# Performance work log

Measured on AMD Instinct MI355X. Metric: run time of the kernel, lower is better.

The kernel has to match this reference:

```python
import jax, jax.numpy as jnp
import numpy as np
import math

B, S, D, H = 1, 2048, 2048, 16
DH, DHID, DKER = 128, 256, 128  # dim_head, dim_hid, dim_ker


def _uniform(k, shape, a):
    return jax.random.uniform(k, shape, jnp.float32, -a, a)


def setup_inputs() -> dict:
    key = jax.random.key(0)
    ks = jax.random.split(key, 14)
    a1 = math.sqrt(6.0 / (DH + DHID))
    a2 = math.sqrt(6.0 / (DKER + DHID))
    a3 = math.sqrt(6.0 / (2 * DKER))
    return {
        "x_t": jax.random.normal(ks[0], (B, S, D), jnp.float32),
        "q": jax.random.normal(ks[1], (B, S, D), jnp.float32),
        "k": jax.random.normal(ks[2], (B, S, D), jnp.float32),
        "v": jax.random.normal(ks[3], (B, S, D), jnp.float32),
        "lr_attn_mask": jax.random.bernoulli(ks[4], 0.5, (B, H, S, S)),
        "sparse_norms_lse": jax.random.normal(ks[5], (B, H, S, 1), jnp.float32),
        "sparse_attn_weights": jax.random.normal(ks[6], (B, H, S, S), jnp.float32),
        "lambda_constant": 0,
        "kernel_q_mat1": _uniform(ks[7], (H, DH, DHID), a1),
        "kernel_k_mat1": _uniform(ks[8], (H, DH, DHID), a1),
        "kernel_q_mat2": _uniform(ks[9], (H, DHID, DKER), a2),
        "kernel_k_mat2": _uniform(ks[10], (H, DHID, DKER), a2),
        "interaction_k": _uniform(ks[11], (H, DKER, DKER), a3),
        "scalingD": jnp.full((1, H, 1, DKER), 1e-4, jnp.float32),
        "scalingD2": jnp.full((1, H, 1, DKER), 1e-4, jnp.float32),
    }


def _gelu(x):
    return jax.nn.gelu(x, approximate=False)  # matches torch F.gelu default


def reference(x_t, q, k, v, lr_attn_mask, sparse_norms_lse, sparse_attn_weights,
              lambda_constant, kernel_q_mat1, kernel_k_mat1, kernel_q_mat2,
              kernel_k_mat2, interaction_k, scalingD, scalingD2):
    Bq, Sq, Dq = q.shape
    dh = Dq // H
    # [B,S,D] -> [B,H,S,dh]
    qh = q.reshape(Bq, Sq, H, dh).transpose(0, 2, 1, 3)
    kh = k.reshape(Bq, Sq, H, dh).transpose(0, 2, 1, 3)
    vh = v.reshape(Bq, Sq, H, dh).transpose(0, 2, 1, 3)

    # per-head two-layer feature maps (dropout is identity at eval)
    qf = _gelu(jnp.einsum('bhsd,hde->bhse', qh, kernel_q_mat1))
    qf = _gelu(jnp.einsum('bhse,hef->bhsf', qf, kernel_q_mat2))
    kf = _gelu(jnp.einsum('bhsd,hde->bhse', kh, kernel_k_mat1))
    kf = jnp.abs(scalingD) * _gelu(jnp.einsum('bhse,hef->bhsf', kf, kernel_k_mat2))
    kf = kf + jnp.einsum('bhse,hef->bhsf', kf, interaction_k) * scalingD2

    # masked non-negative kernel scores [B,H,S,S]
    scores = jnp.einsum('bhse,bhte->bhst', jnp.abs(qf), jnp.abs(kf))
    m = lr_attn_mask.astype(scores.dtype)
    scores = m * scores

    lr_norms_lse = jnp.log(scores.sum(axis=-1, keepdims=True) + 1e-6)
    norm_factor_lse = jnp.logaddexp(lr_norms_lse, sparse_norms_lse)

    logits = jnp.log(scores + 1e-6) * m + (1.0 - m) * sparse_attn_weights
    attn = jnp.exp(logits - norm_factor_lse)

    out = jnp.einsum('bhst,bhtd->bhsd', attn, vh)
    return out.transpose(0, 2, 1, 3).reshape(Bq, Sq, Dq)
```

## Files before the change

### kernel.cpp

```cpp
#include <hip/hip_runtime.h>
#include <hip/hip_bf16.h>
#include <math.h>

#define H_    16
#define S_    2048
#define D_    2048
#define DH_   128
#define DHID_ 256
#define DKER_ 128

typedef __attribute__((ext_vector_type(8))) short short8v;
typedef __attribute__((ext_vector_type(4))) float float4v;
typedef __attribute__((ext_vector_type(4))) int int4v;

static __device__ __forceinline__ short f2bf(float x){
  union { float f; unsigned u; } v; v.f = x;
  unsigned r = v.u + 0x7fffu + ((v.u >> 16) & 1u);
  return (short)(r >> 16);
}
static __device__ __forceinline__ float gelu_f(float x){
  float y = 0.7978845608028654f * (x + 0.044715f * x * x * x);
  float e = __expf(2.0f * y);
  float t = 1.0f - 2.0f / (e + 1.0f);
  return 0.5f * x * (1.0f + t);
}
static __device__ __forceinline__ float4v mfma16(short8v a, short8v b, float4v c){
  return __builtin_amdgcn_mfma_f32_16x16x32_bf16(a, b, c, 0, 0, 0);
}
static __device__ __forceinline__ unsigned cvtpk(float lo, float hi){
  unsigned d;
  asm("v_cvt_pk_bf16_f32 %0, %1, %2" : "=v"(d) : "v"(lo), "v"(hi));
  return d;
}
static __device__ __forceinline__ void glds16(const void* g, void* l){
  __builtin_amdgcn_global_load_lds(
      (const __attribute__((address_space(1))) void*)g,
      (__attribute__((address_space(3))) void*)l, 16, 0, 0);
}

__global__ __launch_bounds__(256) void prep_kernel(
    const void* __restrict__ mask,
    unsigned* __restrict__ MP,
    const float* __restrict__ w1q, short* __restrict__ W1qT,
    const float* __restrict__ w1k, short* __restrict__ W1kT,
    const float* __restrict__ w2q, short* __restrict__ W2qT,
    const float* __restrict__ w2k, short* __restrict__ W2kT,
    const float* __restrict__ ik,  short* __restrict__ IKT,
    const float* __restrict__ v,   short* __restrict__ V2){
  __shared__ float tile[32][33];
  __shared__ int sb, sf, so, sflag;
  int b = blockIdx.x;
  int tid = threadIdx.x;

  if (b < 8192){
    {
      const unsigned* mw = (const unsigned*)mask;
      int bin = 1, f32ok = 1, odd0 = 1;
      for (int i = tid; i < 1024; i += 256){
        unsigned w = mw[i];
        if (w > 1u) bin = 0;
        if (w != 0u && w != 0x3F800000u) f32ok = 0;
        if ((i & 1) && w != 0u) odd0 = 0;
      }
      if (tid == 0){ sb = 1; sf = 1; so = 1; }
      __syncthreads();
      if (!bin)  atomicAnd(&sb, 0);
      if (!f32ok) atomicAnd(&sf, 0);
      if (!odd0) atomicAnd(&so, 0);
      __syncthreads();
      if (tid == 0) sflag = sb ? (so ? 3 : 0) : (sf ? 2 : 1);
      __syncthreads();
    }
    int flag = sflag;
    size_t w = (size_t)b * 256 + tid;
    size_t base = w * 32;
    unsigned bits = 0;
    if (flag == 0){
      const int4v* m = (const int4v*)((const int*)mask + base);
      #pragma unroll
      for (int c = 0; c < 8; ++c){
        int4v x = m[c];
        bits |= (x[0] != 0 ? 1u : 0u) << (c*4+0);
        bits |= (x[1] != 0 ? 1u : 0u) << (c*4+1);
        bits |= (x[2] != 0 ? 1u : 0u) << (c*4+2);
        bits |= (x[3] != 0 ? 1u : 0u) << (c*4+3);
      }
    } else if (flag == 1){
      const int4v* m = (const int4v*)((const unsigned char*)mask + base);
      #pragma unroll
      for (int c = 0; c < 2; ++c){
        int4v x = m[c];
        #pragma unroll
        for (int e = 0; e < 4; ++e){
          unsigned u = (unsigned)x[e];
          #pragma unroll
          for (int bb = 0; bb < 4; ++bb)
            bits |= (((u >> (8*bb)) & 0xffu) != 0 ? 1u : 0u) << (c*16 + e*4 + bb);
        }
      }
    } else if (flag == 2){
      const float4v* m = (const float4v*)((const float*)mask + base);
      #pragma unroll
      for (int c = 0; c < 8; ++c){
        float4v x = m[c];
        bits |= (x[0] != 0.0f ? 1u : 0u) << (c*4+0);
        bits |= (x[1] != 0.0f ? 1u : 0u) << (c*4+1);
        bits |= (x[2] != 0.0f ? 1u : 0u) << (c*4+2);
        bits |= (x[3] != 0.0f ? 1u : 0u) << (c*4+3);
      }
    } else {
      const int4v* m = (const int4v*)((const int*)mask + 2*base);
      #pragma unroll
      for (int c = 0; c < 16; ++c){
        int4v x = m[c];
        bits |= (x[0] != 0 ? 1u : 0u) << (c*2+0);
        bits |= (x[2] != 0 ? 1u : 0u) << (c*2+1);
      }
    }
    MP[w] = bits;
    return;
  }
  b -= 8192;
  if (b < 2048){
    int h = b >> 7, bx = b & 127;
    int d = tid & 127, oct = tid >> 7;
    int t8 = bx * 2 + oct;
    int t32 = t8 >> 2, o = t8 & 3;
    const float* src = v + (size_t)(t32 * 32) * D_ + h * DH_ + d;
    short8v ov;
    #pragma unroll
    for (int j = 0; j < 8; ++j){
      int trel = o * 4 + (j & 3) + ((j >> 2) << 4);
      ov[j] = f2bf(src[(size_t)trel * D_]);
    }
    *(short8v*)(V2 + (((size_t)h * (S_/8) + t8) * DH_ + d) * 8) = ov;
    return;
  }
  b -= 2048;
  const float* src; short* dst; int R, C, bx, by, h;
  if (b < 512){        src = w1q; dst = W1qT; R = DH_;  C = DHID_;
                       bx = b & 7; by = (b >> 3) & 3; h = b >> 5; }
  else if (b < 1024){  b -= 512;  src = w1k; dst = W1kT; R = DH_;  C = DHID_;
                       bx = b & 7; by = (b >> 3) & 3; h = b >> 5; }
  else if (b < 1536){  b -= 1024; src = w2q; dst = W2qT; R = DHID_; C = DKER_;
                       bx = b & 3; by = (b >> 2) & 7; h = b >> 5; }
  else if (b < 2048){  b -= 1536; src = w2k; dst = W2kT; R = DHID_; C = DKER_;
                       bx = b & 3; by = (b >> 2) & 7; h = b >> 5; }
  else {               b -= 2048; src = ik;  dst = IKT;  R = DKER_; C = DKER_;
                       bx = b & 3; by = (b >> 2) & 3; h = b >> 4; }
  int tx = tid & 31, ty = tid >> 5;
  int c0 = bx * 32, r0 = by * 32;
  const float* s = src + (size_t)h * R * C;
  short* d = dst + (size_t)h * R * C;
  #pragma unroll
  for (int i = 0; i < 32; i += 8)
    tile[ty + i][tx] = s[(size_t)(r0 + ty + i) * C + (c0 + tx)];
  __syncthreads();
  #pragma unroll
  for (int i = 0; i < 32; i += 8)
    d[(size_t)(c0 + ty + i) * R + (r0 + tx)] = f2bf(tile[tx][ty + i]);
}

__global__ __launch_bounds__(256) void feat_kernel(
    const float* __restrict__ q, const float* __restrict__ k,
    const short* __restrict__ W1qT, const short* __restrict__ W2qT,
    const short* __restrict__ W1kT, const short* __restrict__ W2kT,
    const short* __restrict__ IKT, const float* __restrict__ sD,
    const float* __restrict__ sD2,
    short* __restrict__ QF, short* __restrict__ KF){
  __shared__ __align__(16) short yls[4][16][264];
  int z = blockIdx.y;
  bool isq = z < 16;
  int h = z & 15;
  const float* X = isq ? q : k;
  const short* W1T = isq ? W1qT : W1kT;
  const short* W2T = isq ? W2qT : W2kT;
  int lane = threadIdx.x & 63, warp = threadIdx.x >> 6;
  int s0 = (blockIdx.x * 4 + warp) * 16;
  int col = lane & 15, rg = lane >> 4;
  short8v a[4];
  {
    const float* xr = X + (size_t)(s0 + col) * D_ + h * DH_;
    #pragma unroll
    for (int kb = 0; kb < 4; ++kb){
      int k0 = kb * 32 + rg * 8;
      float4v x0 = *(const float4v*)(xr + k0);
      float4v x1 = *(const float4v*)(xr + k0 + 4);
      union { unsigned u[4]; short8v v8; } t;
      t.u[0] = cvtpk(x0[0], x0[1]); t.u[1] = cvtpk(x0[2], x0[3]);
      t.u[2] = cvtpk(x1[0], x1[1]); t.u[3] = cvtpk(x1[2], x1[3]);
      a[kb] = t.v8;
    }
  }
  const short* wbase = W1T + (size_t)h * DHID_ * DH_;
  #pragma unroll
  for (int j = 0; j < 16; ++j){
    int n = j * 16;
    float4v c = {0.f, 0.f, 0.f, 0.f};
    const short* wr = wbase + (size_t)(n + col) * DH_ + rg * 8;
    #pragma unroll
    for (int kb = 0; kb < 4; ++kb)
      c = mfma16(a[kb], *(const short8v*)(wr + kb * 32), c);
    #pragma unroll
    for (int r = 0; r < 4; ++r)
      yls[warp][rg * 4 + r][n + col] = f2bf(gelu_f(c[r]));
  }
  short8v a2[8];
  #pragma unroll
  for (int kb = 0; kb < 8; ++kb)
    a2[kb] = *(const short8v*)(&yls[warp][col][kb * 32 + rg * 8]);
  const short* wb2 = W2T + (size_t)h * DKER_ * DHID_;

  if (isq){
    short* qb = QF + ((size_t)h * S_ + s0) * DKER_;
    #pragma unroll
    for (int j = 0; j < 8; ++j){
      int n = j * 16;
      float4v c = {0.f, 0.f, 0.f, 0.f};
      const short* wr = wb2 + (size_t)(n + col) * DHID_ + rg * 8;
      #pragma unroll
      for (int kb = 0; kb < 8; ++kb)
        c = mfma16(a2[kb], *(const short8v*)(wr + kb * 32), c);
      #pragma unroll
      for (int r = 0; r < 4; ++r)
        qb[(size_t)(rg * 4 + r) * DKER_ + n + col] = f2bf(fabsf(gelu_f(c[r])));
    }
    return;
  }
  float kf0[8][4];
  #pragma unroll
  for (int j = 0; j < 8; ++j){
    int n = j * 16;
    float4v c = {0.f, 0.f, 0.f, 0.f};
    const short* wr = wb2 + (size_t)(n + col) * DHID_ + rg * 8;
    #pragma unroll
    for (int kb = 0; kb < 8; ++kb)
      c = mfma16(a2[kb], *(const short8v*)(wr + kb * 32), c);
    float sc = fabsf(sD[h * DKER_ + n + col]);
    #pragma unroll
    for (int r = 0; r < 4; ++r) kf0[j][r] = sc * gelu_f(c[r]);
  }
  #pragma unroll
  for (int j = 0; j < 8; ++j)
    #pragma unroll
    for (int r = 0; r < 4; ++r)
      yls[warp][rg * 4 + r][j * 16 + col] = f2bf(kf0[j][r]);
  short8v pa[4];
  #pragma unroll
  for (int kb = 0; kb < 4; ++kb)
    pa[kb] = *(const short8v*)(&yls[warp][col][kb * 32 + rg * 8]);
  const short* ib = IKT + (size_t)h * DKER_ * DKER_;
  short* ko = KF + ((size_t)h * S_ + s0) * DKER_;
  #pragma unroll
  for (int j = 0; j < 8; ++j){
    int n = j * 16;
    float4v c = {0.f, 0.f, 0.f, 0.f};
    const short* ir = ib + (size_t)(n + col) * DKER_ + rg * 8;
    #pragma unroll
    for (int kb = 0; kb < 4; ++kb)
      c = mfma16(pa[kb], *(const short8v*)(ir + kb * 32), c);
    float s2 = sD2[h * DKER_ + n + col];
    #pragma unroll
    for (int r = 0; r < 4; ++r)
      ko[(size_t)(rg * 4 + r) * DKER_ + n + col] = f2bf(fabsf(kf0[j][r] + c[r] * s2));
  }
}

__global__ __launch_bounds__(512, 4) void main_attn_kernel(
    const short* __restrict__ QF, const short* __restrict__ KF,
    const short* __restrict__ V2, const unsigned* __restrict__ MP,
    const float* __restrict__ SW, const float* __restrict__ LSE,
    float* __restrict__ OUT){
  __shared__ __align__(16) char smem[65536];
  int tid = threadIdx.x;
  int lane = tid & 63, warp = tid >> 6;
  int hf = warp >> 2, w4 = warp & 3;
  int flat = blockIdx.y * 32 + blockIdx.x;
  int nf = (flat & 7) * 64 + (flat >> 3);
  int sblk = nf & 31, h = nf >> 5;
  int tbase = hf * (S_ / 2);
  int s0 = (sblk * 4 + w4) * 16;
  int col = lane & 15, rg = lane >> 4;

  short* kbuf = (short*)(smem + hf * 32768);
  short* vbuf = (short*)(smem + hf * 32768 + 16384);

  short8v qa[4];
  const short* qr = QF + ((size_t)h * S_ + s0 + col) * DKER_ + rg * 8;
  #pragma unroll
  for (int kb = 0; kb < 4; ++kb) qa[kb] = *(const short8v*)(qr + kb * 32);

  float4v acc[8];
  #pragma unroll
  for (int j = 0; j < 8; ++j) acc[j] = (float4v){0.f, 0.f, 0.f, 0.f};
  float rs = 0.f;

  const char* kf_base = (const char*)(KF + ((size_t)h * S_ + tbase) * DKER_);
  const char* v2_base = (const char*)(V2 + ((size_t)h * (S_/8) + (tbase >> 3)) * DH_ * 8);
  int c0 = w4 * 64 + lane, c1 = c0 + 256;
  int kg0 = (c0 * 16) ^ (((c0 >> 4) & 7) << 4);
  int kg1 = (c1 * 16) ^ (((c1 >> 4) & 7) << 4);
  int vg0 = c0 * 16, vg1 = c1 * 16;
  int lds_lo = w4 * 512, lds_hi = 2048 + w4 * 512;

  const float* swrow = SW + ((size_t)h * S_ + s0 + col) * S_ + tbase + rg * 4;
  const unsigned* mpr = MP + ((size_t)h * S_ + s0 + col) * (S_ / 32) + (tbase >> 5);

  {
    glds16(kf_base + kg0, &kbuf[lds_lo]);
    glds16(kf_base + kg1, &kbuf[lds_hi]);
    glds16(v2_base + vg0, &vbuf[lds_lo]);
    glds16(v2_base + vg1, &vbuf[lds_hi]);
  }
  __syncthreads();

  int swz = (col & 7) << 4;
  int rowb0 = col * 256 + rg * 16;
  const int NITER = (S_ / 2) / 32;

  for (int ti = 0; ti < NITER; ++ti){
    int cur = ti & 1;
    if (ti + 1 < NITER){
      const char* kt = kf_base + (size_t)(ti + 1) * 8192;
      const char* vt = v2_base + (size_t)(ti + 1) * 8192;
      glds16(kt + kg0, &kbuf[(cur ^ 1) * 4096 + lds_lo]);
      glds16(kt + kg1, &kbuf[(cur ^ 1) * 4096 + lds_hi]);
      glds16(vt + vg0, &vbuf[(cur ^ 1) * 4096 + lds_lo]);
      glds16(vt + vg1, &vbuf[(cur ^ 1) * 4096 + lds_hi]);
    }
    const char* kbp = (const char*)kbuf + cur * 8192;
    const char* vbp = (const char*)vbuf + cur * 8192;

    float4v q0 = {0.f,0.f,0.f,0.f}, q1 = {0.f,0.f,0.f,0.f};
    #pragma unroll
    for (int kk = 0; kk < 4; ++kk){
      short8v a0 = *(const short8v*)(kbp + ((rowb0 + kk * 64) ^ swz));
      short8v a1 = *(const short8v*)(kbp + ((rowb0 + 4096 + kk * 64) ^ swz));
      q0 = mfma16(a0, qa[kk], q0);
      q1 = mfma16(a1, qa[kk], q1);
    }

    const float* swp = swrow + ti * 32;
    float4v sv0 = *(const float4v*)swp;
    float4v sv1 = *(const float4v*)(swp + 16);
    unsigned mw = mpr[ti];
    float p0[4], p1[4];
    #pragma unroll
    for (int r = 0; r < 4; ++r){
      bool m0 = (mw >> (rg * 4 + r)) & 1u;
      bool m1 = (mw >> (16 + rg * 4 + r)) & 1u;
      p0[r] = m0 ? (q0[r] + 1e-6f) : __expf(sv0[r]);
      p1[r] = m1 ? (q1[r] + 1e-6f) : __expf(sv1[r]);
      if (m0) rs += q0[r];
      if (m1) rs += q1[r];
    }
    union { unsigned u[4]; short8v v8; } pw;
    pw.u[0] = cvtpk(p0[0], p0[1]); pw.u[1] = cvtpk(p0[2], p0[3]);
    pw.u[2] = cvtpk(p1[0], p1[1]); pw.u[3] = cvtpk(p1[2], p1[3]);
    short8v pa = pw.v8;

    #pragma unroll
    for (int j = 0; j < 8; ++j){
      short8v vf = *(const short8v*)(vbp + rg * 2048 + (j * 16 + col) * 16);
      acc[j] = mfma16(pa, vf, acc[j]);
    }
    __syncthreads();
  }

  rs += __shfl_xor(rs, 16);
  rs += __shfl_xor(rs, 32);

  __syncthreads();
  float* cb = (float*)smem;
  float* rb = (float*)(smem + 32768);
  if (hf == 1){
    float* cw = cb + (size_t)w4 * 16 * 128;
    #pragma unroll
    for (int j = 0; j < 8; ++j)
      #pragma unroll
      for (int r = 0; r < 4; ++r)
        cw[(size_t)(rg * 4 + r) * 128 + j * 16 + col] = acc[j][r];
    if (lane < 16) rb[w4 * 16 + lane] = rs;
  }
  __syncthreads();
  if (hf == 0){
    float* cw = cb + (size_t)w4 * 16 * 128;
    #pragma unroll
    for (int j = 0; j < 8; ++j)
      #pragma unroll
      for (int r = 0; r < 4; ++r)
        acc[j][r] += cw[(size_t)(rg * 4 + r) * 128 + j * 16 + col];
    rs += rb[w4 * 16 + col];

    float a = logf(rs + 1e-6f);
    float b = LSE[h * S_ + s0 + col];
    float mx = fmaxf(a, b);
    float sc_col = expf(-(mx + log1pf(expf(-fabsf(a - b)))));
    float scale[4];
    #pragma unroll
    for (int r = 0; r < 4; ++r) scale[r] = __shfl(sc_col, rg * 4 + r);
    float* ob = OUT + (size_t)s0 * D_ + h * DH_;
    #pragma unroll
    for (int j = 0; j < 8; ++j)
      #pragma unroll
      for (int r = 0; r < 4; ++r)
        ob[(size_t)(rg * 4 + r) * D_ + j * 16 + col] = acc[j][r] * scale[r];
  }
}

extern "C" void kernel_launch(void* const* d_in, const int* in_sizes, int n_in,
                              void* d_out, int out_size, void* d_ws, size_t ws_size,
                              hipStream_t stream){
  (void)in_sizes; (void)n_in; (void)out_size; (void)ws_size;
  const float* q   = (const float*)d_in[1];
  const float* k   = (const float*)d_in[2];
  const float* v   = (const float*)d_in[3];
  const void*  msk = d_in[4];
  const float* lse = (const float*)d_in[5];
  const float* sw  = (const float*)d_in[6];
  const float* w1q = (const float*)d_in[8];
  const float* w1k = (const float*)d_in[9];
  const float* w2q = (const float*)d_in[10];
  const float* w2k = (const float*)d_in[11];
  const float* ik  = (const float*)d_in[12];
  const float* sD  = (const float*)d_in[13];
  const float* sD2 = (const float*)d_in[14];
  float* out = (float*)d_out;

  char* ws = (char*)d_ws;
  size_t o = 0;
  o += 256;
  short* W1qT = (short*)(ws + o);      o += (size_t)H_ * DHID_ * DH_ * 2;
  short* W1kT = (short*)(ws + o);      o += (size_t)H_ * DHID_ * DH_ * 2;
  short* W2qT = (short*)(ws + o);      o += (size_t)H_ * DKER_ * DHID_ * 2;
  short* W2kT = (short*)(ws + o);      o += (size_t)H_ * DKER_ * DHID_ * 2;
  short* IKT  = (short*)(ws + o);      o += (size_t)H_ * DKER_ * DKER_ * 2;
  short* V2   = (short*)(ws + o);      o += (size_t)S_ * D_ * 2;
  short* QFb  = (short*)(ws + o);      o += (size_t)H_ * S_ * DKER_ * 2;
  short* KFb  = (short*)(ws + o);      o += (size_t)H_ * S_ * DKER_ * 2;
  unsigned* MP = (unsigned*)(ws + o);  o += (size_t)H_ * S_ * (S_/32) * 4;

  prep_kernel<<<12544, 256, 0, stream>>>(msk, MP,
      w1q, W1qT, w1k, W1kT, w2q, W2qT, w2k, W2kT, ik, IKT, v, V2);

  feat_kernel<<<dim3(S_/64, 32), 256, 0, stream>>>(q, k,
      W1qT, W2qT, W1kT, W2kT, IKT, sD, sD2, QFb, KFb);

  main_attn_kernel<<<dim3(32, 16), 512, 0, stream>>>(
      QFb, KFb, V2, MP, sw, lse, out);
}
```

Measured before the change: 244.8 us.

## Read raw attention mask directly in attention loop instead of bit-packing pass

Drops the separate prep stage that packed the boolean mask into bitwords, and has the main attention kernel detect the mask dtype per wave and read raw mask elements inside the key loop through a templated loop. This removes one full write and read of the packed mask buffer and a large chunk of prep-kernel blocks. In exchange, the attention kernel now streams the unpacked mask (1–8 bytes per element) alongside the sparse weights, which raises its per-iteration global traffic.

```diff
diff --git a/kernel.cpp b/kernel.cpp
--- a/kernel.cpp
+++ b/kernel.cpp
@@ -39,8 +39,6 @@
 }
 
 __global__ __launch_bounds__(256) void prep_kernel(
-    const void* __restrict__ mask,
-    unsigned* __restrict__ MP,
     const float* __restrict__ w1q, short* __restrict__ W1qT,
     const float* __restrict__ w1k, short* __restrict__ W1kT,
     const float* __restrict__ w2q, short* __restrict__ W2qT,
@@ -48,79 +46,9 @@
     const float* __restrict__ ik,  short* __restrict__ IKT,
     const float* __restrict__ v,   short* __restrict__ V2){
   __shared__ float tile[32][33];
-  __shared__ int sb, sf, so, sflag;
   int b = blockIdx.x;
   int tid = threadIdx.x;
 
-  if (b < 8192){
-    {
-      const unsigned* mw = (const unsigned*)mask;
-      int bin = 1, f32ok = 1, odd0 = 1;
-      for (int i = tid; i < 1024; i += 256){
-        unsigned w = mw[i];
-        if (w > 1u) bin = 0;
-        if (w != 0u && w != 0x3F800000u) f32ok = 0;
-        if ((i & 1) && w != 0u) odd0 = 0;
-      }
-      if (tid == 0){ sb = 1; sf = 1; so = 1; }
-      __syncthreads();
-      if (!bin)  atomicAnd(&sb, 0);
-      if (!f32ok) atomicAnd(&sf, 0);
-      if (!odd0) atomicAnd(&so, 0);
-      __syncthreads();
-      if (tid == 0) sflag = sb ? (so ? 3 : 0) : (sf ? 2 : 1);
-      __syncthreads();
-    }
-    int flag = sflag;
-    size_t w = (size_t)b * 256 + tid;
-    size_t base = w * 32;
-    unsigned bits = 0;
-    if (flag == 0){
-      const int4v* m = (const int4v*)((const int*)mask + base);
-      #pragma unroll
-      for (int c = 0; c < 8; ++c){
-        int4v x = m[c];
-        bits |= (x[0] != 0 ? 1u : 0u) << (c*4+0);
-        bits |= (x[1] != 0 ? 1u : 0u) << (c*4+1);
-        bits |= (x[2] != 0 ? 1u : 0u) << (c*4+2);
-        bits |= (x[3] != 0 ? 1u : 0u) << (c*4+3);
-      }
-    } else if (flag == 1){
-      const int4v* m = (const int4v*)((const unsigned char*)mask + base);
-      #pragma unroll
-      for (int c = 0; c < 2; ++c){
-        int4v x = m[c];
-        #pragma unroll
-        for (int e = 0; e < 4; ++e){
-          unsigned u = (unsigned)x[e];
-          #pragma unroll
-          for (int bb = 0; bb < 4; ++bb)
-            bits |= (((u >> (8*bb)) & 0xffu) != 0 ? 1u : 0u) << (c*16 + e*4 + bb);
-        }
-      }
-    } else if (flag == 2){
-      const float4v* m = (const float4v*)((const float*)mask + base);
-      #pragma unroll
-      for (int c = 0; c < 8; ++c){
-        float4v x = m[c];
-        bits |= (x[0] != 0.0f ? 1u : 0u) << (c*4+0);
-        bits |= (x[1] != 0.0f ? 1u : 0u) << (c*4+1);
-        bits |= (x[2] != 0.0f ? 1u : 0u) << (c*4+2);
-        bits |= (x[3] != 0.0f ? 1u : 0u) << (c*4+3);
-      }
-    } else {
-      const int4v* m = (const int4v*)((const int*)mask + 2*base);
-      #pragma unroll
-      for (int c = 0; c < 16; ++c){
-        int4v x = m[c];
-        bits |= (x[0] != 0 ? 1u : 0u) << (c*2+0);
-        bits |= (x[2] != 0 ? 1u : 0u) << (c*2+1);
-      }
-    }
-    MP[w] = bits;
-    return;
-  }
-  b -= 8192;
   if (b < 2048){
     int h = b >> 7, bx = b & 127;
     int d = tid & 127, oct = tid >> 7;
@@ -266,9 +194,97 @@
   }
 }
 
+template<int MT>
+static __device__ __forceinline__ void attn_tloop(
+    const char* __restrict__ mrow0, const float* __restrict__ swrow,
+    const char* __restrict__ kf_base, const char* __restrict__ v2_base,
+    short* kbuf, short* vbuf,
+    int kg0, int kg1, int vg0, int vg1, int lds_lo, int lds_hi,
+    int swz, int rowb0, int rg, int col,
+    const short8v (&qa)[4], float4v (&acc)[8], float& rs){
+  const int NITER = (S_ / 2) / 32;
+  for (int ti = 0; ti < NITER; ++ti){
+    int cur = ti & 1;
+    if (ti + 1 < NITER){
+      const char* kt = kf_base + (size_t)(ti + 1) * 8192;
+      const char* vt = v2_base + (size_t)(ti + 1) * 8192;
+      glds16(kt + kg0, &kbuf[(cur ^ 1) * 4096 + lds_lo]);
+      glds16(kt + kg1, &kbuf[(cur ^ 1) * 4096 + lds_hi]);
+      glds16(vt + vg0, &vbuf[(cur ^ 1) * 4096 + lds_lo]);
+      glds16(vt + vg1, &vbuf[(cur ^ 1) * 4096 + lds_hi]);
+    }
+    const char* kbp = (const char*)kbuf + cur * 8192;
+    const char* vbp = (const char*)vbuf + cur * 8192;
+
+    float4v q0 = {0.f,0.f,0.f,0.f}, q1 = {0.f,0.f,0.f,0.f};
+    #pragma unroll
+    for (int kk = 0; kk < 4; ++kk){
+      short8v a0 = *(const short8v*)(kbp + ((rowb0 + kk * 64) ^ swz));
+      short8v a1 = *(const short8v*)(kbp + ((rowb0 + 4096 + kk * 64) ^ swz));
+      q0 = mfma16(a0, qa[kk], q0);
+      q1 = mfma16(a1, qa[kk], q1);
+    }
+
+    const float* swp = swrow + ti * 32;
+    float4v sv0 = *(const float4v*)swp;
+    float4v sv1 = *(const float4v*)(swp + 16);
+
+    bool m0[4], m1[4];
+    if constexpr (MT == 0){
+      const int* mp = (const int*)(mrow0 + (size_t)ti * 128);
+      int4v x0 = *(const int4v*)mp;
+      int4v x1 = *(const int4v*)(mp + 16);
+      #pragma unroll
+      for (int r = 0; r < 4; ++r){ m0[r] = x0[r] != 0; m1[r] = x1[r] != 0; }
+    } else if constexpr (MT == 1){
+      const unsigned* mp = (const unsigned*)(mrow0 + (size_t)ti * 32);
+      unsigned x0 = mp[0], x1 = mp[4];
+      #pragma unroll
+      for (int r = 0; r < 4; ++r){
+        m0[r] = ((x0 >> (8*r)) & 0xffu) != 0u;
+        m1[r] = ((x1 >> (8*r)) & 0xffu) != 0u;
+      }
+    } else if constexpr (MT == 2){
+      const float* mp = (const float*)(mrow0 + (size_t)ti * 128);
+      float4v x0 = *(const float4v*)mp;
+      float4v x1 = *(const float4v*)(mp + 16);
+      #pragma unroll
+      for (int r = 0; r < 4; ++r){ m0[r] = x0[r] != 0.0f; m1[r] = x1[r] != 0.0f; }
+    } else {
+      const int* mp = (const int*)(mrow0 + (size_t)ti * 256);
+      int4v xa = *(const int4v*)mp;
+      int4v xb = *(const int4v*)(mp + 4);
+      int4v xc = *(const int4v*)(mp + 32);
+      int4v xd = *(const int4v*)(mp + 36);
+      m0[0] = xa[0] != 0; m0[1] = xa[2] != 0; m0[2] = xb[0] != 0; m0[3] = xb[2] != 0;
+      m1[0] = xc[0] != 0; m1[1] = xc[2] != 0; m1[2] = xd[0] != 0; m1[3] = xd[2] != 0;
+    }
+
+    float p0[4], p1[4];
+    #pragma unroll
+    for (int r = 0; r < 4; ++r){
+      p0[r] = m0[r] ? (q0[r] + 1e-6f) : __expf(sv0[r]);
+      p1[r] = m1[r] ? (q1[r] + 1e-6f) : __expf(sv1[r]);
+      if (m0[r]) rs += q0[r];
+      if (m1[r]) rs += q1[r];
+    }
+    union { unsigned u[4]; short8v v8; } pw;
+    pw.u[0] = cvtpk(p0[0], p0[1]); pw.u[1] = cvtpk(p0[2], p0[3]);
+    pw.u[2] = cvtpk(p1[0], p1[1]); pw.u[3] = cvtpk(p1[2], p1[3]);
+    short8v pa = pw.v8;
+
+    #pragma unroll
+    for (int j = 0; j < 8; ++j){
+      short8v vf = *(const short8v*)(vbp + rg * 2048 + (j * 16 + col) * 16);
+      acc[j] = mfma16(pa, vf, acc[j]);
+    }
+    __syncthreads();
+  }
+}
+
 __global__ __launch_bounds__(512, 4) void main_attn_kernel(
     const short* __restrict__ QF, const short* __restrict__ KF,
-    const short* __restrict__ V2, const unsigned* __restrict__ MP,
+    const short* __restrict__ V2, const void* __restrict__ MSK,
     const float* __restrict__ SW, const float* __restrict__ LSE,
     float* __restrict__ OUT){
   __shared__ __align__(16) char smem[65536];
@@ -304,68 +320,44 @@
   int lds_lo = w4 * 512, lds_hi = 2048 + w4 * 512;
 
   const float* swrow = SW + ((size_t)h * S_ + s0 + col) * S_ + tbase + rg * 4;
-  const unsigned* mpr = MP + ((size_t)h * S_ + s0 + col) * (S_ / 32) + (tbase >> 5);
-
+
+  glds16(kf_base + kg0, &kbuf[lds_lo]);
+  glds16(kf_base + kg1, &kbuf[lds_hi]);
+  glds16(v2_base + vg0, &vbuf[lds_lo]);
+  glds16(v2_base + vg1, &vbuf[lds_hi]);
+
+  int flag;
   {
-    glds16(kf_base + kg0, &kbuf[lds_lo]);
-    glds16(kf_base + kg1, &kbuf[lds_hi]);
-    glds16(v2_base + vg0, &vbuf[lds_lo]);
-    glds16(v2_base + vg1, &vbuf[lds_hi]);
+    const unsigned* mw = (const unsigned*)MSK;
+    int bin = 1, f32ok = 1, odd0 = 1;
+    #pragma unroll
+    for (int i = 0; i < 16; ++i){
+      unsigned w = mw[lane + i * 64];
+      if (w > 1u) bin = 0;
+      if (w != 0u && w != 0x3F800000u) f32ok = 0;
+      if (((lane + i * 64) & 1) && w != 0u) odd0 = 0;
+    }
+    bin = __all(bin); odd0 = __all(odd0); f32ok = __all(f32ok);
+    flag = bin ? (odd0 ? 3 : 0) : (f32ok ? 2 : 1);
   }
   __syncthreads();
 
   int swz = (col & 7) << 4;
   int rowb0 = col * 256 + rg * 16;
-  const int NITER = (S_ / 2) / 32;
-
-  for (int ti = 0; ti < NITER; ++ti){
-    int cur = ti & 1;
-    if (ti + 1 < NITER){
-      const char* kt = kf_base + (size_t)(ti + 1) * 8192;
-      const char* vt = v2_base + (size_t)(ti + 1) * 8192;
-      glds16(kt + kg0, &kbuf[(cur ^ 1) * 4096 + lds_lo]);
-      glds16(kt + kg1, &kbuf[(cur ^ 1) * 4096 + lds_hi]);
-      glds16(vt + vg0, &vbuf[(cur ^ 1) * 4096 + lds_lo]);
-      glds16(vt + vg1, &vbuf[(cur ^ 1) * 4096 + lds_hi]);
-    }
-    const char* kbp = (const char*)kbuf + cur * 8192;
-    const char* vbp = (const char*)vbuf + cur * 8192;
-
-    float4v q0 = {0.f,0.f,0.f,0.f}, q1 = {0.f,0.f,0.f,0.f};
-    #pragma unroll
-    for (int kk = 0; kk < 4; ++kk){
-      short8v a0 = *(const short8v*)(kbp + ((rowb0 + kk * 64) ^ swz));
-      short8v a1 = *(const short8v*)(kbp + ((rowb0 + 4096 + kk * 64) ^ swz));
-      q0 = mfma16(a0, qa[kk], q0);
-      q1 = mfma16(a1, qa[kk], q1);
-    }
-
-    const float* swp = swrow + ti * 32;
-    float4v sv0 = *(const float4v*)swp;
-    float4v sv1 = *(const float4v*)(swp + 16);
-    unsigned mw = mpr[ti];
-    float p0[4], p1[4];
-    #pragma unroll
-    for (int r = 0; r < 4; ++r){
-      bool m0 = (mw >> (rg * 4 + r)) & 1u;
-      bool m1 = (mw >> (16 + rg * 4 + r)) & 1u;
-      p0[r] = m0 ? (q0[r] + 1e-6f) : __expf(sv0[r]);
-      p1[r] = m1 ? (q1[r] + 1e-6f) : __expf(sv1[r]);
-      if (m0) rs += q0[r];
-      if (m1) rs += q1[r];
-    }
-    union { unsigned u[4]; short8v v8; } pw;
-    pw.u[0] = cvtpk(p0[0], p0[1]); pw.u[1] = cvtpk(p0[2], p0[3]);
-    pw.u[2] = cvtpk(p1[0], p1[1]); pw.u[3] = cvtpk(p1[2], p1[3]);
-    short8v pa = pw.v8;
-
-    #pragma unroll
-    for (int j = 0; j < 8; ++j){
-      short8v vf = *(const short8v*)(vbp + rg * 2048 + (j * 16 + col) * 16);
-      acc[j] = mfma16(pa, vf, acc[j]);
-    }
-    __syncthreads();
-  }
+  size_t e0 = ((size_t)h * S_ + s0 + col) * S_ + tbase + rg * 4;
+
+  if (flag == 0)
+    attn_tloop<0>((const char*)MSK + e0 * 4, swrow, kf_base, v2_base, kbuf, vbuf,
+                  kg0, kg1, vg0, vg1, lds_lo, lds_hi, swz, rowb0, rg, col, qa, acc, rs);
+  else if (flag == 1)
+    attn_tloop<1>((const char*)MSK + e0, swrow, kf_base, v2_base, kbuf, vbuf,
+                  kg0, kg1, vg0, vg1, lds_lo, lds_hi, swz, rowb0, rg, col, qa, acc, rs);
+  else if (flag == 2)
+    attn_tloop<2>((const char*)MSK + e0 * 4, swrow, kf_base, v2_base, kbuf, vbuf,
+                  kg0, kg1, vg0, vg1, lds_lo, lds_hi, swz, rowb0, rg, col, qa, acc, rs);
+  else
+    attn_tloop<3>((const char*)MSK + e0 * 8, swrow, kf_base, v2_base, kbuf, vbuf,
+                  kg0, kg1, vg0, vg1, lds_lo, lds_hi, swz, rowb0, rg, col, qa, acc, rs);
 
   rs += __shfl_xor(rs, 16);
   rs += __shfl_xor(rs, 32);
@@ -438,14 +430,13 @@
   short* V2   = (short*)(ws + o);      o += (size_t)S_ * D_ * 2;
   short* QFb  = (short*)(ws + o);      o += (size_t)H_ * S_ * DKER_ * 2;
   short* KFb  = (short*)(ws + o);      o += (size_t)H_ * S_ * DKER_ * 2;
-  unsigned* MP = (unsigned*)(ws + o);  o += (size_t)H_ * S_ * (S_/32) * 4;
-
-  prep_kernel<<<12544, 256, 0, stream>>>(msk, MP,
+
+  prep_kernel<<<4352, 256, 0, stream>>>(
       w1q, W1qT, w1k, W1kT, w2q, W2qT, w2k, W2kT, ik, IKT, v, V2);
 
   feat_kernel<<<dim3(S_/64, 32), 256, 0, stream>>>(q, k,
       W1qT, W2qT, W1kT, W2kT, IKT, sD, sD2, QFb, KFb);
 
   main_attn_kernel<<<dim3(32, 16), 512, 0, stream>>>(
-      QFb, KFb, V2, MP, sw, lse, out);
-}
+      QFb, KFb, V2, msk, sw, lse, out);
+}
```

Measured after the change: 234.9 us (median of 2 runs). 4.0% less time.
